# Optimization experiments

Hardware: AMD Instinct MI355X
Metric: run time of the kernel (lower is better)

## Reference

```python
import jax, jax.numpy as jnp
import numpy as np


def setup_inputs() -> dict:
    key = jax.random.key(0)
    k1, k2 = jax.random.split(key)
    n_rows, cols, n_values = 4096, 2048, 16
    x = jax.random.normal(k1, (n_rows, cols), dtype=jnp.float32)
    values = jax.random.normal(k2, (n_rows, n_values), dtype=jnp.float32)
    return {"x": x, "values": values}


def reference(x, values):
    # x: [R, C], values: [R, V] (per-row codebook)
    # distances: [R, C, V] broadcast squared distance
    distances = (x[:, :, None] - values[:, None, :]) ** 2
    min_indices = jnp.argmin(distances, axis=-1)          # [R, C]
    # gather nearest codebook value per row
    selected = jnp.take_along_axis(values, min_indices, axis=1)  # [R, C]
    return selected
```

## Files before the change

### kernel.cpp

```cpp
#include <hip/hip_runtime.h>
#include <math.h>


#define N_ROWS 4096
#define N_COLS 2048
#define N_VALS 16

typedef float f32x4 __attribute__((ext_vector_type(4)));

struct Entry { float v; int idx; };

__global__ __launch_bounds__(256) void vq_rowcodebook_kernel(
    const float* __restrict__ x,
    const float* __restrict__ values,
    float* __restrict__ out)
{
    const int row = blockIdx.x;
    const float* vr = values + (size_t)row * N_VALS;
    const int tid = threadIdx.x;

    __shared__ Entry arr[N_VALS + 1];

    if (tid < N_VALS) {
        const float vi = vr[tid];
        int rank = 0;
#pragma unroll
        for (int j = 0; j < N_VALS; ++j) {
            const float vj = vr[j];
            rank += (vj < vi || (vj == vi && j < tid)) ? 1 : 0;
        }
        arr[rank].v = vi;
        arr[rank].idx = tid;
        if (tid == 0) { arr[N_VALS].v = INFINITY; arr[N_VALS].idx = 0x7fffffff; }
    }
    __syncthreads();

    const float p4 = arr[4].v, p8 = arr[8].v, p12 = arr[12].v;
    const char* base = (const char*)arr;

    const f32x4* xr   = (const f32x4*)(x   + (size_t)row * N_COLS);
    f32x4*       outr = (f32x4*)      (out + (size_t)row * N_COLS);

#pragma unroll
    for (int it = 0; it < 2; ++it) {
        const int j = tid + it * 256;
        const f32x4 xv = xr[j];

        f32x4 o;
#pragma unroll
        for (int e = 0; e < 4; ++e) {
            const float xe = xv[e];

            const bool b1 = (p8 <= xe);
            int posB = b1 ? 64 : 0;
            const float pv2 = b1 ? p12 : p4;
            posB += (pv2 <= xe) ? 32 : 0;
            posB += (*(const float*)(base + posB + 16) <= xe) ? 16 : 0;
            posB += (*(const float*)(base + posB + 8)  <= xe) ? 8  : 0;

            const Entry L = *(const Entry*)(base + posB);
            const Entry R = *(const Entry*)(base + posB + 8);

            const float tL = xe - L.v;
            const float tR = xe - R.v;
            const float dL = tL * tL;
            const float dR = tR * tR;
            const bool takeL = (dL < dR) | ((dL == dR) & (L.idx < R.idx));
            o[e] = takeL ? L.v : R.v;
        }
        outr[j] = o;
    }
}

extern "C" void kernel_launch(void* const* d_in, const int* in_sizes, int n_in,
                              void* d_out, int out_size, void* d_ws, size_t ws_size,
                              hipStream_t stream) {
    const float* x      = (const float*)d_in[0];
    const float* values = (const float*)d_in[1];
    float* out          = (float*)d_out;

    vq_rowcodebook_kernel<<<N_ROWS, 256, 0, stream>>>(x, values, out);
}
```

Baseline: 83.38 us.

## Precompute exact decision thresholds between sorted codebook values via bit-level bisection

Each row now computes exact float decision boundaries between adjacent sorted codebook entries, using a binary search over the ordered bit representation that reproduces the squared-distance and tie-break rule. The per-element work shrinks to a 4-step threshold search plus one LDS load of the chosen value, dropping the final two-entry distance comparison. In exchange there is an extra setup phase per block, with up to about 32 bisection iterations on 15 threads, and a second barrier. It is memory bound, so the gain is likely small.

```diff
diff --git a/kernel.cpp b/kernel.cpp
--- a/kernel.cpp
+++ b/kernel.cpp
@@ -8,7 +8,12 @@
 
 typedef float f32x4 __attribute__((ext_vector_type(4)));
 
-struct Entry { float v; int idx; };
+__device__ __forceinline__ unsigned ford(unsigned u) {
+    return (u & 0x80000000u) ? ~u : (u | 0x80000000u);
+}
+__device__ __forceinline__ unsigned funord(unsigned o) {
+    return (o & 0x80000000u) ? (o & 0x7fffffffu) : ~o;
+}
 
 __global__ __launch_bounds__(256) void vq_rowcodebook_kernel(
     const float* __restrict__ x,
@@ -19,7 +24,8 @@
     const float* vr = values + (size_t)row * N_VALS;
     const int tid = threadIdx.x;
 
-    __shared__ Entry arr[N_VALS + 1];
+    __shared__ float LUT[32];
+    __shared__ int   SIDX[16];
 
     if (tid < N_VALS) {
         const float vi = vr[tid];
@@ -29,14 +35,37 @@
             const float vj = vr[j];
             rank += (vj < vi || (vj == vi && j < tid)) ? 1 : 0;
         }
-        arr[rank].v = vi;
-        arr[rank].idx = tid;
-        if (tid == 0) { arr[N_VALS].v = INFINITY; arr[N_VALS].idx = 0x7fffffff; }
+        LUT[16 + rank] = vi;
+        SIDX[rank] = tid;
+        if (tid == 0) LUT[0] = -INFINITY;
     }
     __syncthreads();
 
-    const float p4 = arr[4].v, p8 = arr[8].v, p12 = arr[12].v;
-    const char* base = (const char*)arr;
+    if (tid >= 1 && tid < N_VALS) {
+        const float a = LUT[16 + tid - 1];
+        const float b = LUT[16 + tid];
+        const int  ia = SIDX[tid - 1];
+        const int  ib = SIDX[tid];
+        unsigned L = ford(__float_as_uint(a));
+        unsigned H = ford(__float_as_uint(b)) + 1u;
+        while (L < H) {
+            const unsigned M = L + ((H - L) >> 1);
+            const float xm = __uint_as_float(funord(M));
+            const float tL = xm - a;
+            const float tR = xm - b;
+            const float dL = tL * tL;
+            const float dR = tR * tR;
+            const bool takeR = (dR < dL) || ((dR == dL) && (ib < ia));
+            if (takeR) H = M; else L = M + 1;
+        }
+        LUT[tid] = __uint_as_float(funord(L));
+    }
+    __syncthreads();
+
+    const float t8  = LUT[8];
+    const float t4  = LUT[4];
+    const float t12 = LUT[12];
+    const char* base = (const char*)LUT;
 
     const f32x4* xr   = (const f32x4*)(x   + (size_t)row * N_COLS);
     f32x4*       outr = (f32x4*)      (out + (size_t)row * N_COLS);
@@ -51,22 +80,14 @@
         for (int e = 0; e < 4; ++e) {
             const float xe = xv[e];
 
-            const bool b1 = (p8 <= xe);
-            int posB = b1 ? 64 : 0;
-            const float pv2 = b1 ? p12 : p4;
-            posB += (pv2 <= xe) ? 32 : 0;
-            posB += (*(const float*)(base + posB + 16) <= xe) ? 16 : 0;
-            posB += (*(const float*)(base + posB + 8)  <= xe) ? 8  : 0;
+            const bool b1 = (t8 <= xe);
+            int posB = b1 ? 32 : 0;
+            const float tq = b1 ? t12 : t4;
+            posB += (tq <= xe) ? 16 : 0;
+            posB += (*(const float*)(base + posB + 8) <= xe) ? 8 : 0;
+            posB += (*(const float*)(base + posB + 4) <= xe) ? 4 : 0;
 
-            const Entry L = *(const Entry*)(base + posB);
-            const Entry R = *(const Entry*)(base + posB + 8);
-
-            const float tL = xe - L.v;
-            const float tR = xe - R.v;
-            const float dL = tL * tL;
-            const float dR = tR * tR;
-            const bool takeL = (dL < dR) | ((dL == dR) & (L.idx < R.idx));
-            o[e] = takeL ? L.v : R.v;
+            o[e] = *(const float*)(base + posB + 64);
         }
         outr[j] = o;
     }
```

Result: slower. 86.51 us (+3.7%).
